# Performance work log

Hardware: AMD Instinct MI355X
Metric: run time of the kernel (lower is better)

Reference implementation:

```python
import jax, jax.numpy as jnp
import numpy as np

B, C, H, W = 8, 320, 32, 32
HEADS, DHEAD = 8, 40
CTX_LEN, CTX_DIM = 77, 768
FF_INNER = 4 * C
GROUPS = 32
HW = H * W


def setup_inputs() -> dict:
    key = jax.random.key(0)
    ks = jax.random.split(key, 16)
    def nrm(k, shape, s=0.02):
        return (jax.random.normal(k, shape) * s).astype(jnp.float32)
    z = lambda *s: jnp.zeros(s, jnp.float32)
    o = lambda *s: jnp.ones(s, jnp.float32)
    inp = {}
    inp["x"] = jax.random.normal(ks[0], (B, C, H, W), jnp.float32)
    inp["context"] = jax.random.normal(ks[1], (B, CTX_LEN, CTX_DIM), jnp.float32)
    inp["vis_mask"] = jax.random.uniform(ks[2], (B, HW, HW)) > 0.5
    inp["v2t_mask"] = jax.random.uniform(ks[3], (B, HW, CTX_LEN)) > 0.5
    inp["gn_scale"] = o(C); inp["gn_bias"] = z(C)
    inp["proj_in_w"] = nrm(ks[4], (C, C)); inp["proj_in_b"] = z(C)
    inp["n1_s"] = o(C); inp["n1_b"] = z(C)
    inp["wq1"] = nrm(ks[5], (C, C)); inp["wk1"] = nrm(ks[6], (C, C)); inp["wv1"] = nrm(ks[7], (C, C))
    inp["wo1"] = nrm(ks[8], (C, C)); inp["bo1"] = z(C)
    inp["n2_s"] = o(C); inp["n2_b"] = z(C)
    inp["wq2"] = nrm(ks[9], (C, C)); inp["wk2"] = nrm(ks[10], (CTX_DIM, C)); inp["wv2"] = nrm(ks[11], (CTX_DIM, C))
    inp["wo2"] = nrm(ks[12], (C, C)); inp["bo2"] = z(C)
    inp["n3_s"] = o(C); inp["n3_b"] = z(C)
    inp["ff_w1"] = nrm(ks[13], (C, 2 * FF_INNER)); inp["ff_b1"] = z(2 * FF_INNER)
    inp["ff_w2"] = nrm(ks[14], (FF_INNER, C)); inp["ff_b2"] = z(C)
    inp["proj_out_w"] = nrm(ks[15], (C, C)); inp["proj_out_b"] = z(C)
    return inp


def group_norm(x, scale, bias, eps=1e-6):
    b, c, h, w = x.shape
    xg = x.reshape(b, GROUPS, -1)
    mu = xg.mean(-1, keepdims=True)
    var = xg.var(-1, keepdims=True)
    xn = ((xg - mu) * jax.lax.rsqrt(var + eps)).reshape(b, c, h, w)
    return xn * scale[None, :, None, None] + bias[None, :, None, None]


def layer_norm(x, s, b, eps=1e-5):
    mu = x.mean(-1, keepdims=True)
    var = x.var(-1, keepdims=True)
    return (x - mu) * jax.lax.rsqrt(var + eps) * s + b


def mha(xq, ctx, wq, wk, wv, wo, bo, mask):
    # CrossAttention: manual einsum softmax with boolean mask broadcast over heads
    b, n, _ = xq.shape
    m = ctx.shape[1]
    split = lambda t: t.reshape(b, -1, HEADS, DHEAD).transpose(0, 2, 1, 3)
    q = split(xq @ wq)   # [b,h,n,d]
    k = split(ctx @ wk)  # [b,h,m,d]
    v = split(ctx @ wv)
    sim = jnp.einsum('bhid,bhjd->bhij', q, k) * (DHEAD ** -0.5)
    if mask is not None:
        sim = jnp.where(mask[:, None, :, :], sim, jnp.finfo(sim.dtype).min)
    attn = jax.nn.softmax(sim, axis=-1)
    out = jnp.einsum('bhij,bhjd->bhid', attn, v)
    out = out.transpose(0, 2, 1, 3).reshape(b, n, HEADS * DHEAD)
    return out @ wo + bo


def reference(x, context, vis_mask, v2t_mask, gn_scale, gn_bias, proj_in_w, proj_in_b,
              n1_s, n1_b, wq1, wk1, wv1, wo1, bo1,
              n2_s, n2_b, wq2, wk2, wv2, wo2, bo2,
              n3_s, n3_b, ff_w1, ff_b1, ff_w2, ff_b2,
              proj_out_w, proj_out_b):
    x_in = x
    h = group_norm(x, gn_scale, gn_bias)
    # 1x1 conv proj_in == per-pixel linear; flatten b c h w -> b (hw) c
    h = h.reshape(B, C, HW).transpose(0, 2, 1) @ proj_in_w + proj_in_b
    # masked self-attention (vis mask)
    h = h + mha(layer_norm(h, n1_s, n1_b), layer_norm(h, n1_s, n1_b),
                wq1, wk1, wv1, wo1, bo1, vis_mask)
    # masked cross-attention to text (v2t mask)
    h = h + mha(layer_norm(h, n2_s, n2_b), context,
                wq2, wk2, wv2, wo2, bo2, v2t_mask)
    # GEGLU feedforward (glu=True, mult=4)
    y = layer_norm(h, n3_s, n3_b) @ ff_w1 + ff_b1
    a, g = jnp.split(y, 2, axis=-1)
    h = h + (a * jax.nn.gelu(g, approximate=False)) @ ff_w2 + ff_b2
    # proj_out + residual
    out = (h @ proj_out_w + proj_out_b).transpose(0, 2, 1).reshape(B, C, H, W)
    return out + x_in
```

## Files before the change

kernel.cpp:

```cpp
#include <hip/hip_runtime.h>
#include <hip/hip_bf16.h>
#include <math.h>


#define Bsz   8
#define Cch   320
#define HW    1024
#define NTOK  (Bsz*HW)
#define HEADS 8
#define DHEAD 40
#define CTXL  77
#define CTXD  768
#define FFI   1280
#define MCTX  (Bsz*CTXL)
#define MCTXP 640

typedef unsigned short u16;
typedef unsigned long long u64;
typedef __attribute__((ext_vector_type(8))) u16    u16x8;
typedef __attribute__((ext_vector_type(8))) __bf16 bf16x8;
typedef __attribute__((ext_vector_type(4))) float  f32x4;

__device__ inline u16 f2b(float f) {
    unsigned u = __float_as_uint(f);
    return (u16)((u + 0x7FFFu + ((u >> 16) & 1u)) >> 16);
}

__global__ __launch_bounds__(256) void gn_stats(
    const float* __restrict__ x, const float* __restrict__ scale,
    const float* __restrict__ bias, float* __restrict__ gnA,
    float* __restrict__ gnB)
{
    int blk = blockIdx.x;
    int b = blk >> 5, g = blk & 31;
    int tid = threadIdx.x;
    __shared__ float rs[256], rq[256];
    const float4* xg = (const float4*)(x + ((size_t)b*Cch + g*10)*HW);
    float s = 0.f, q = 0.f;
    #pragma unroll
    for (int i = 0; i < 10; ++i) {
        float4 v = xg[tid + i*256];
        s += v.x + v.y + v.z + v.w;
        q += v.x*v.x + v.y*v.y + v.z*v.z + v.w*v.w;
    }
    rs[tid] = s; rq[tid] = q; __syncthreads();
    for (int off = 128; off > 0; off >>= 1) {
        if (tid < off) { rs[tid] += rs[tid+off]; rq[tid] += rq[tid+off]; }
        __syncthreads();
    }
    if (tid < 10) {
        float mean = rs[0] * (1.f/10240.f);
        float var  = rq[0] * (1.f/10240.f) - mean*mean;
        float inv  = rsqrtf(var + 1e-6f);
        int ch = g*10 + tid;
        float a = inv * scale[ch];
        gnA[b*Cch + ch] = a;
        gnB[b*Cch + ch] = bias[ch] - mean*a;
    }
}

__global__ __launch_bounds__(256) void gn_apply(
    const float* __restrict__ x, const float* __restrict__ gnA,
    const float* __restrict__ gnB, u16* __restrict__ out)
{
    __shared__ u16 T[64*72];
    const int tid = threadIdx.x;
    const int c0 = blockIdx.x * 64;
    const int p0 = blockIdx.y * 64;
    const int b  = blockIdx.z;
    for (int e = tid; e < 512; e += 256) {
        int r = e >> 3, ch = e & 7;
        const float* src = x + ((size_t)(b*Cch + c0 + r))*HW + p0 + ch*8;
        float a  = gnA[b*Cch + c0 + r];
        float bb = gnB[b*Cch + c0 + r];
        float4 v0 = *(const float4*)src;
        float4 v1 = *(const float4*)(src + 4);
        u16x8 val;
        val[0] = f2b(v0.x*a + bb); val[1] = f2b(v0.y*a + bb);
        val[2] = f2b(v0.z*a + bb); val[3] = f2b(v0.w*a + bb);
        val[4] = f2b(v1.x*a + bb); val[5] = f2b(v1.y*a + bb);
        val[6] = f2b(v1.z*a + bb); val[7] = f2b(v1.w*a + bb);
        *(u16x8*)&T[r*72 + (ch ^ (r & 7))*8] = val;
    }
    __syncthreads();
    for (int e = tid; e < 4096; e += 256) {
        int p = e >> 6, c = e & 63;
        u16 v = T[c*72 + (((p >> 3) ^ (c & 7))*8) + (p & 7)];
        out[((size_t)(b*HW + p0 + p))*Cch + c0 + c] = v;
    }
}

__global__ __launch_bounds__(256) void layernorm_kernel(
    const float* __restrict__ in, const float* __restrict__ s,
    const float* __restrict__ bgain, u16* __restrict__ out)
{
    int t = blockIdx.x*4 + (threadIdx.x >> 6);
    int lane = threadIdx.x & 63;
    const float* row = in + (size_t)t*Cch;
    float v[5];
    float sum = 0.f, sq = 0.f;
    #pragma unroll
    for (int i = 0; i < 5; ++i) {
        v[i] = row[lane + 64*i];
        sum += v[i]; sq += v[i]*v[i];
    }
    #pragma unroll
    for (int off = 32; off > 0; off >>= 1) {
        sum += __shfl_xor(sum, off);
        sq  += __shfl_xor(sq,  off);
    }
    float mean = sum * (1.f/320.f);
    float var  = sq  * (1.f/320.f) - mean*mean;
    float inv  = rsqrtf(var + 1e-5f);
    u16* orow = out + (size_t)t*Cch;
    #pragma unroll
    for (int i = 0; i < 5; ++i) {
        int c = lane + 64*i;
        orow[c] = f2b((v[i]-mean)*inv*s[c] + bgain[c]);
    }
}

struct WDesc { const float* src; u16* dst; int K; int N; int nelem; float scl; };
struct WPack { WDesc w[12]; };

#define WBLK 9920
#define CBLK 1920

__global__ __launch_bounds__(256) void preamble(
    WPack p, const float* __restrict__ ctxsrc, u16* __restrict__ ctxdst,
    const void* __restrict__ vis, const void* __restrict__ v2t,
    u64* __restrict__ bvis, u64* __restrict__ bv2t)
{
    int blk = blockIdx.x;
    int tid = threadIdx.x;
    if (blk < WBLK) {
        int idx = blk*256 + tid;
        #pragma unroll
        for (int i = 0; i < 12; ++i) {
            if (idx < p.w[i].nelem) {
                int K = p.w[i].K, N = p.w[i].N;
                int n = idx / K, k = idx - n*K;
                p.w[i].dst[(size_t)n*K + k] =
                    f2b(p.w[i].src[(size_t)k*N + n] * p.w[i].scl);
                return;
            }
            idx -= p.w[i].nelem;
        }
        return;
    }
    if (blk < WBLK + CBLK) {
        int idx = (blk - WBLK)*256 + tid;
        int r = idx / CTXD;
        float v = (r < MCTX) ? ctxsrc[idx] : 0.f;
        ctxdst[idx] = f2b(v);
        return;
    }
    __shared__ int any;
    if (tid == 0) any = 0;
    __syncthreads();
    const unsigned char* probe = (const unsigned char*)vis;
    for (int i = tid; i < 4096; i += 256)
        if ((i & 3) && probe[i]) any = 1;
    __syncthreads();
    const int isU8 = any;
    int mb = blk - WBLK - CBLK;
    const void* mask; u64* bits; int Lkv, nw;
    if (mb < 2048) { mask = vis; bits = bvis; Lkv = HW;   nw = 16; }
    else           { mask = v2t; bits = bv2t; Lkv = CTXL; nw = 2; mb -= 2048; }
    const int wv = tid >> 6, lane = tid & 63;
    const int row = mb*4 + wv;
    const unsigned char* m8  = (const unsigned char*)mask;
    const int*           m32 = (const int*)mask;
    const size_t base = (size_t)row * Lkv;
    for (int w = 0; w < nw; ++w) {
        int j = w*64 + lane;
        bool on = (j < Lkv) && (isU8 ? (m8[base+j] != 0) : (m32[base+j] != 0));
        u64 word = __ballot(on);
        if (lane == 0) bits[(size_t)row*nw + w] = word;
    }
}

__global__ __launch_bounds__(256) void gemm_bf16(
    const u16* __restrict__ A, const u16* __restrict__ Wt,
    const float* __restrict__ bias, const float* __restrict__ res,
    float* __restrict__ out, u16* __restrict__ out_bf, int M, int N, int K)
{
    __shared__ u16 As[2][128*40];
    __shared__ u16 Bs[2][64*40];
    const int tid  = threadIdx.x;
    const int lane = tid & 63;
    const int w    = tid >> 6;
    const int m0   = blockIdx.y * 128;
    const int n0   = blockIdx.x * 64;
    const int fr   = lane & 15, fg = lane >> 4;
    const int ar   = tid >> 2, ac = tid & 3;

    const u16* pa0 = A  + (size_t)(m0 + ar)*K      + ac*8;
    const u16* pa1 = A  + (size_t)(m0 + ar + 64)*K + ac*8;
    const u16* pb  = Wt + (size_t)(n0 + ar)*K      + ac*8;
    const int nk = K >> 5;

    *(u16x8*)&As[0][ar*40 + ac*8]      = *(const u16x8*)pa0;
    *(u16x8*)&As[0][(ar+64)*40 + ac*8] = *(const u16x8*)pa1;
    *(u16x8*)&Bs[0][ar*40 + ac*8]      = *(const u16x8*)pb;
    u16x8 ra0, ra1, rb;
    if (nk > 1) {
        pa0 += 32; pa1 += 32; pb += 32;
        ra0 = *(const u16x8*)pa0;
        ra1 = *(const u16x8*)pa1;
        rb  = *(const u16x8*)pb;
    }

    f32x4 acc[2][4] = {};
    for (int i = 0; i < nk; ++i) {
        __syncthreads();
        const int cur = i & 1;
        if (i + 1 < nk) {
            *(u16x8*)&As[cur^1][ar*40 + ac*8]      = ra0;
            *(u16x8*)&As[cur^1][(ar+64)*40 + ac*8] = ra1;
            *(u16x8*)&Bs[cur^1][ar*40 + ac*8]      = rb;
            if (i + 2 < nk) {
                pa0 += 32; pa1 += 32; pb += 32;
                ra0 = *(const u16x8*)pa0;
                ra1 = *(const u16x8*)pa1;
                rb  = *(const u16x8*)pb;
            }
        }
        bf16x8 a0 = *(const bf16x8*)&As[cur][(w*32      + fr)*40 + fg*8];
        bf16x8 a1 = *(const bf16x8*)&As[cur][(w*32 + 16 + fr)*40 + fg*8];
        #pragma unroll
        for (int nt = 0; nt < 4; ++nt) {
            bf16x8 b = *(const bf16x8*)&Bs[cur][(nt*16 + fr)*40 + fg*8];
            acc[0][nt] = __builtin_amdgcn_mfma_f32_16x16x32_bf16(a0, b, acc[0][nt], 0, 0, 0);
            acc[1][nt] = __builtin_amdgcn_mfma_f32_16x16x32_bf16(a1, b, acc[1][nt], 0, 0, 0);
        }
    }
    #pragma unroll
    for (int at = 0; at < 2; ++at) {
        #pragma unroll
        for (int nt = 0; nt < 4; ++nt) {
            int gn = n0 + nt*16 + fr;
            float bv = bias ? bias[gn] : 0.f;
            #pragma unroll
            for (int i = 0; i < 4; ++i) {
                int gm = m0 + w*32 + at*16 + fg*4 + i;
                float v = acc[at][nt][i] + bv;
                if (res) v += res[(size_t)gm*N + gn];
                if (out) out[(size_t)gm*N + gn] = v;
                if (out_bf) out_bf[(size_t)gm*N + gn] = f2b(v);
            }
        }
    }
}

__global__ __launch_bounds__(256) void gemm_pout(
    const u16* __restrict__ A, const u16* __restrict__ Wt,
    const float* __restrict__ bias, const float* __restrict__ x,
    float* __restrict__ out, int K)
{
    __shared__ u16 As[2][128*40];
    __shared__ u16 Bs[2][64*40];
    const int tid  = threadIdx.x;
    const int lane = tid & 63;
    const int w    = tid >> 6;
    const int m0   = blockIdx.y * 128;
    const int n0   = blockIdx.x * 64;
    const int fr   = lane & 15, fg = lane >> 4;
    const int ar   = tid >> 2, ac = tid & 3;

    const u16* pa0 = A  + (size_t)(m0 + ar)*K      + ac*8;
    const u16* pa1 = A  + (size_t)(m0 + ar + 64)*K + ac*8;
    const u16* pb  = Wt + (size_t)(n0 + ar)*K      + ac*8;
    const int nk = K >> 5;

    *(u16x8*)&As[0][ar*40 + ac*8]      = *(const u16x8*)pa0;
    *(u16x8*)&As[0][(ar+64)*40 + ac*8] = *(const u16x8*)pa1;
    *(u16x8*)&Bs[0][ar*40 + ac*8]      = *(const u16x8*)pb;
    u16x8 ra0, ra1, rb;
    if (nk > 1) {
        pa0 += 32; pa1 += 32; pb += 32;
        ra0 = *(const u16x8*)pa0;
        ra1 = *(const u16x8*)pa1;
        rb  = *(const u16x8*)pb;
    }

    f32x4 acc[2][4] = {};
    for (int i = 0; i < nk; ++i) {
        __syncthreads();
        const int cur = i & 1;
        if (i + 1 < nk) {
            *(u16x8*)&As[cur^1][ar*40 + ac*8]      = ra0;
            *(u16x8*)&As[cur^1][(ar+64)*40 + ac*8] = ra1;
            *(u16x8*)&Bs[cur^1][ar*40 + ac*8]      = rb;
            if (i + 2 < nk) {
                pa0 += 32; pa1 += 32; pb += 32;
                ra0 = *(const u16x8*)pa0;
                ra1 = *(const u16x8*)pa1;
                rb  = *(const u16x8*)pb;
            }
        }
        bf16x8 a0 = *(const bf16x8*)&As[cur][(w*32      + fr)*40 + fg*8];
        bf16x8 a1 = *(const bf16x8*)&As[cur][(w*32 + 16 + fr)*40 + fg*8];
        #pragma unroll
        for (int nt = 0; nt < 4; ++nt) {
            bf16x8 b = *(const bf16x8*)&Bs[cur][(nt*16 + fr)*40 + fg*8];
            acc[0][nt] = __builtin_amdgcn_mfma_f32_16x16x32_bf16(a0, b, acc[0][nt], 0, 0, 0);
            acc[1][nt] = __builtin_amdgcn_mfma_f32_16x16x32_bf16(a1, b, acc[1][nt], 0, 0, 0);
        }
    }
    #pragma unroll
    for (int at = 0; at < 2; ++at) {
        #pragma unroll
        for (int nt = 0; nt < 4; ++nt) {
            int gn = n0 + nt*16 + fr;
            float bv = bias[gn];
            int gm0 = m0 + w*32 + at*16 + fg*4;
            int b   = gm0 >> 10;
            int p   = gm0 & (HW-1);
            size_t o = ((size_t)(b*Cch + gn))*HW + p;
            f32x4 xv = *(const f32x4*)&x[o];
            f32x4 vv;
            #pragma unroll
            for (int i = 0; i < 4; ++i) vv[i] = acc[at][nt][i] + bv + xv[i];
            *(f32x4*)&out[o] = vv;
        }
    }
}

__global__ __launch_bounds__(256) void ctx_kv_gemm(
    const u16* __restrict__ ctx, const u16* __restrict__ wk,
    const u16* __restrict__ wv, u16* __restrict__ kout, u16* __restrict__ vout)
{
    __shared__ u16 As[2][64*40];
    __shared__ u16 Bs[2][64*40];
    const int tid  = threadIdx.x;
    const int lane = tid & 63;
    const int w    = tid >> 6;
    const int m0   = blockIdx.y * 64;
    const int n0   = blockIdx.x * 64;
    const u16* Wt  = blockIdx.z ? wv : wk;
    u16* outp      = blockIdx.z ? vout : kout;
    const int fr   = lane & 15, fg = lane >> 4;
    const int ar   = tid >> 2, ac = tid & 3;

    const u16* pa = ctx + (size_t)(m0 + ar)*CTXD + ac*8;
    const u16* pb = Wt  + (size_t)(n0 + ar)*CTXD + ac*8;
    const int nk = CTXD >> 5;

    *(u16x8*)&As[0][ar*40 + ac*8] = *(const u16x8*)pa;
    *(u16x8*)&Bs[0][ar*40 + ac*8] = *(const u16x8*)pb;
    u16x8 ra, rb;
    pa += 32; pb += 32;
    ra = *(const u16x8*)pa;
    rb = *(const u16x8*)pb;

    f32x4 acc[4] = {};
    for (int i = 0; i < nk; ++i) {
        __syncthreads();
        const int cur = i & 1;
        if (i + 1 < nk) {
            *(u16x8*)&As[cur^1][ar*40 + ac*8] = ra;
            *(u16x8*)&Bs[cur^1][ar*40 + ac*8] = rb;
            if (i + 2 < nk) {
                pa += 32; pb += 32;
                ra = *(const u16x8*)pa;
                rb = *(const u16x8*)pb;
            }
        }
        bf16x8 a = *(const bf16x8*)&As[cur][(w*16 + fr)*40 + fg*8];
        #pragma unroll
        for (int nt = 0; nt < 4; ++nt) {
            bf16x8 b = *(const bf16x8*)&Bs[cur][(nt*16 + fr)*40 + fg*8];
            acc[nt] = __builtin_amdgcn_mfma_f32_16x16x32_bf16(a, b, acc[nt], 0, 0, 0);
        }
    }
    #pragma unroll
    for (int nt = 0; nt < 4; ++nt) {
        int gn = n0 + nt*16 + fr;
        #pragma unroll
        for (int i = 0; i < 4; ++i) {
            int gm = m0 + w*16 + fg*4 + i;
            if (gm < MCTX)
                outp[(size_t)gm*Cch + gn] = f2b(acc[nt][i]);
        }
    }
}

__global__ __launch_bounds__(256) void geglu_bf16(
    const u16* __restrict__ A, const u16* __restrict__ Wt,
    const float* __restrict__ b1, u16* __restrict__ out, int M, int K)
{
    __shared__ u16 As[2][128*40];
    __shared__ u16 Ba[2][64*40];
    __shared__ u16 Bg[2][64*40];
    const int tid  = threadIdx.x;
    const int lane = tid & 63;
    const int w    = tid >> 6;
    const int m0   = blockIdx.y * 128;
    const int n0   = blockIdx.x * 64;
    const int fr   = lane & 15, fg = lane >> 4;
    const int ar   = tid >> 2, ac = tid & 3;

    const u16* pa0 = A  + (size_t)(m0 + ar)*K      + ac*8;
    const u16* pa1 = A  + (size_t)(m0 + ar + 64)*K + ac*8;
    const u16* pba = Wt + (size_t)(n0 + ar)*K       + ac*8;
    const u16* pbg = Wt + (size_t)(FFI + n0 + ar)*K + ac*8;
    const int nk = K >> 5;

    *(u16x8*)&As[0][ar*40 + ac*8]      = *(const u16x8*)pa0;
    *(u16x8*)&As[0][(ar+64)*40 + ac*8] = *(const u16x8*)pa1;
    *(u16x8*)&Ba[0][ar*40 + ac*8]      = *(const u16x8*)pba;
    *(u16x8*)&Bg[0][ar*40 + ac*8]      = *(const u16x8*)pbg;
    u16x8 ra0, ra1, rba, rbg;
    if (nk > 1) {
        pa0 += 32; pa1 += 32; pba += 32; pbg += 32;
        ra0 = *(const u16x8*)pa0;
        ra1 = *(const u16x8*)pa1;
        rba = *(const u16x8*)pba;
        rbg = *(const u16x8*)pbg;
    }

    f32x4 aca[2][4] = {}, acg[2][4] = {};
    for (int i = 0; i < nk; ++i) {
        __syncthreads();
        const int cur = i & 1;
        if (i + 1 < nk) {
            *(u16x8*)&As[cur^1][ar*40 + ac*8]      = ra0;
            *(u16x8*)&As[cur^1][(ar+64)*40 + ac*8] = ra1;
            *(u16x8*)&Ba[cur^1][ar*40 + ac*8]      = rba;
            *(u16x8*)&Bg[cur^1][ar*40 + ac*8]      = rbg;
            if (i + 2 < nk) {
                pa0 += 32; pa1 += 32; pba += 32; pbg += 32;
                ra0 = *(const u16x8*)pa0;
                ra1 = *(const u16x8*)pa1;
                rba = *(const u16x8*)pba;
                rbg = *(const u16x8*)pbg;
            }
        }
        bf16x8 a0 = *(const bf16x8*)&As[cur][(w*32      + fr)*40 + fg*8];
        bf16x8 a1 = *(const bf16x8*)&As[cur][(w*32 + 16 + fr)*40 + fg*8];
        #pragma unroll
        for (int nt = 0; nt < 4; ++nt) {
            bf16x8 ba = *(const bf16x8*)&Ba[cur][(nt*16 + fr)*40 + fg*8];
            bf16x8 bg = *(const bf16x8*)&Bg[cur][(nt*16 + fr)*40 + fg*8];
            aca[0][nt] = __builtin_amdgcn_mfma_f32_16x16x32_bf16(a0, ba, aca[0][nt], 0, 0, 0);
            aca[1][nt] = __builtin_amdgcn_mfma_f32_16x16x32_bf16(a1, ba, aca[1][nt], 0, 0, 0);
            acg[0][nt] = __builtin_amdgcn_mfma_f32_16x16x32_bf16(a0, bg, acg[0][nt], 0, 0, 0);
            acg[1][nt] = __builtin_amdgcn_mfma_f32_16x16x32_bf16(a1, bg, acg[1][nt], 0, 0, 0);
        }
    }
    #pragma unroll
    for (int at = 0; at < 2; ++at) {
        #pragma unroll
        for (int nt = 0; nt < 4; ++nt) {
            int gn = n0 + nt*16 + fr;
            float ba = b1[gn], bg = b1[FFI + gn];
            #pragma unroll
            for (int i = 0; i < 4; ++i) {
                int gm = m0 + w*32 + at*16 + fg*4 + i;
                float av = aca[at][nt][i] + ba;
                float gv = acg[at][nt][i] + bg;
                float gel = 0.5f*gv*(1.f + erff(gv*0.70710678118654752f));
                out[(size_t)gm*FFI + gn] = f2b(av*gel);
            }
        }
    }
}

__global__ __launch_bounds__(256) void transpose_v(
    const u16* __restrict__ in, int istride, u16* __restrict__ out,
    int Ltok, int ostride)
{
    __shared__ u16 T[64*72];
    const int tid = threadIdx.x;
    const int c0 = blockIdx.x * 64;
    const int t0 = blockIdx.y * 64;
    const int b  = blockIdx.z;
    for (int e = tid; e < 512; e += 256) {
        int r = e >> 3, ch = e & 7;
        u16x8 val = {};
        if (t0 + r < Ltok)
            val = *(const u16x8*)(in + ((size_t)(b*Ltok + t0 + r))*istride + c0 + ch*8);
        *(u16x8*)&T[r*72 + (ch ^ (r & 7))*8] = val;
    }
    __syncthreads();
    for (int e = tid; e < 4096; e += 256) {
        int c = e >> 6, t = e & 63;
        u16 v = T[t*72 + (((c >> 3) ^ (t & 7))*8) + (c & 7)];
        out[((size_t)(b*Cch + c0 + c))*ostride + t0 + t] = v;
    }
}

__global__ __launch_bounds__(256) void flash_mfma(
    const u16* __restrict__ qb, int qstride,
    const u16* __restrict__ kb, int kstride,
    const u16* __restrict__ vt, int vstride,
    const u64* __restrict__ mbits, int nw,
    u16* __restrict__ out,
    int Lkv)
{
    __shared__ u16 QPs[64*72];
    __shared__ u16 Ks[64*72];
    __shared__ u16 Vs[48*72];

    const int tid  = threadIdx.x;
    const int lane = tid & 63;
    const int w    = tid >> 6;
    const int col  = lane & 15;
    const int quad = lane >> 4;
    const int q0   = blockIdx.x * 64;
    const int h    = blockIdx.y;
    const int b    = blockIdx.z;
    const int ch   = tid & 7;
    const int r0   = tid >> 3;

    {
        const u16* qT = qb + ((size_t)(b*HW + q0))*qstride + (size_t)h*DHEAD + ch*8;
        u16x8 v0 = {}, v1 = {};
        if (ch < 5) {
            v0 = *(const u16x8*)(qT + (size_t)r0*qstride);
            v1 = *(const u16x8*)(qT + (size_t)(r0+32)*qstride);
        }
        *(u16x8*)&QPs[r0*72 + ch*8]      = v0;
        *(u16x8*)&QPs[(r0+32)*72 + ch*8] = v1;
    }
    __syncthreads();
    const bf16x8 qa0 = *(const bf16x8*)&QPs[(w*16 + col)*72 +  0 + quad*8];
    const bf16x8 qa1 = *(const bf16x8*)&QPs[(w*16 + col)*72 + 32 + quad*8];

    const u16* kT = kb + (size_t)b*Lkv*kstride + (size_t)h*DHEAD + ch*8;
    const bool kok = ch < 5;
    const u16* vT = vt + ((size_t)(b*Cch + h*DHEAD))*vstride + ch*8;
    const u64* mrow = mbits + ((size_t)(b*HW + q0 + w*16 + quad*4))*nw;

    f32x4 acc_o[3] = {};

    const int nkt = (Lkv + 63) / 64;
    for (int jt = 0; jt < nkt; ++jt) {
        const int j0 = jt*64;
        __syncthreads();
        {
            u16x8 v0 = {}, v1 = {};
            if (kok) {
                if (j0 + r0      < Lkv) v0 = *(const u16x8*)(kT + (size_t)(j0 + r0)*kstride);
                if (j0 + r0 + 32 < Lkv) v1 = *(const u16x8*)(kT + (size_t)(j0 + r0 + 32)*kstride);
            }
            *(u16x8*)&Ks[r0*72 + ch*8]      = v0;
            *(u16x8*)&Ks[(r0+32)*72 + ch*8] = v1;
        }
        {
            u16x8 v0 = {};
            if (r0 < DHEAD) v0 = *(const u16x8*)(vT + (size_t)r0*vstride + j0);
            *(u16x8*)&Vs[r0*72 + ch*8] = v0;
            if (tid < 128) {
                int d1 = 32 + (tid >> 3);
                u16x8 v1 = {};
                if (d1 < DHEAD) v1 = *(const u16x8*)(vT + (size_t)d1*vstride + j0);
                else if (d1 == DHEAD) {
                    #pragma unroll
                    for (int z = 0; z < 8; ++z) v1[z] = 0x3F80;
                }
                *(u16x8*)&Vs[d1*72 + ch*8] = v1;
            }
        }
        __syncthreads();

        u64 mw[4];
        #pragma unroll
        for (int i = 0; i < 4; ++i) mw[i] = mrow[i*nw + jt];

        f32x4 s[4] = {};
        #pragma unroll
        for (int nt = 0; nt < 4; ++nt) {
            bf16x8 b0 = *(const bf16x8*)&Ks[(nt*16 + col)*72 +  0 + quad*8];
            bf16x8 b1 = *(const bf16x8*)&Ks[(nt*16 + col)*72 + 32 + quad*8];
            s[nt] = __builtin_amdgcn_mfma_f32_16x16x32_bf16(qa0, b0, s[nt], 0, 0, 0);
            s[nt] = __builtin_amdgcn_mfma_f32_16x16x32_bf16(qa1, b1, s[nt], 0, 0, 0);
        }

        #pragma unroll
        for (int i = 0; i < 4; ++i) {
            #pragma unroll
            for (int nt = 0; nt < 4; ++nt) {
                float p = __expf(s[nt][i]);
                unsigned bits = (unsigned)(mw[i] >> (nt*16));
                s[nt][i] = ((bits >> col) & 1u) ? p : 0.f;
            }
        }

        #pragma unroll
        for (int nt = 0; nt < 4; ++nt)
            #pragma unroll
            for (int i = 0; i < 4; ++i)
                QPs[(w*16 + quad*4 + i)*68 + nt*16 + col] =
                    (u16)(__float_as_uint(s[nt][i]) >> 16);

        bf16x8 pa0, pa1;
        __builtin_memcpy(&pa0, &QPs[(w*16 + col)*68 +  0 + quad*8], 16);
        __builtin_memcpy(&pa1, &QPs[(w*16 + col)*68 + 32 + quad*8], 16);
        #pragma unroll
        for (int nt = 0; nt < 3; ++nt) {
            bf16x8 vb0 = *(const bf16x8*)&Vs[(nt*16 + col)*72 +  0 + quad*8];
            bf16x8 vb1 = *(const bf16x8*)&Vs[(nt*16 + col)*72 + 32 + quad*8];
            acc_o[nt] = __builtin_amdgcn_mfma_f32_16x16x32_bf16(pa0, vb0, acc_o[nt], 0, 0, 0);
            acc_o[nt] = __builtin_amdgcn_mfma_f32_16x16x32_bf16(pa1, vb1, acc_o[nt], 0, 0, 0);
        }
    }

    float inv_l[4];
    #pragma unroll
    for (int i = 0; i < 4; ++i)
        inv_l[i] = 1.f / __shfl(acc_o[2][i], (lane & 48) | 8);

    #pragma unroll
    for (int nt = 0; nt < 3; ++nt) {
        int d = nt*16 + col;
        if (d < DHEAD) {
            #pragma unroll
            for (int i = 0; i < 4; ++i) {
                int q = q0 + w*16 + quad*4 + i;
                out[((size_t)(b*HW + q))*Cch + h*DHEAD + d] = f2b(acc_o[nt][i] * inv_l[i]);
            }
        }
    }
}

extern "C" void kernel_launch(void* const* d_in, const int* in_sizes, int n_in,
                              void* d_out, int out_size, void* d_ws, size_t ws_size,
                              hipStream_t stream)
{
    const float* x        = (const float*)d_in[0];
    const float* context  = (const float*)d_in[1];
    const void*  vis_mask = d_in[2];
    const void*  v2t_mask = d_in[3];
    const float* gn_s     = (const float*)d_in[4];
    const float* gn_b     = (const float*)d_in[5];
    const float* proj_in_w= (const float*)d_in[6];
    const float* proj_in_b= (const float*)d_in[7];
    const float* n1_s     = (const float*)d_in[8];
    const float* n1_b     = (const float*)d_in[9];
    const float* wq1      = (const float*)d_in[10];
    const float* wk1      = (const float*)d_in[11];
    const float* wv1      = (const float*)d_in[12];
    const float* wo1      = (const float*)d_in[13];
    const float* bo1      = (const float*)d_in[14];
    const float* n2_s     = (const float*)d_in[15];
    const float* n2_b     = (const float*)d_in[16];
    const float* wq2      = (const float*)d_in[17];
    const float* wk2      = (const float*)d_in[18];
    const float* wv2      = (const float*)d_in[19];
    const float* wo2      = (const float*)d_in[20];
    const float* bo2      = (const float*)d_in[21];
    const float* n3_s     = (const float*)d_in[22];
    const float* n3_b     = (const float*)d_in[23];
    const float* ff_w1    = (const float*)d_in[24];
    const float* ff_b1    = (const float*)d_in[25];
    const float* ff_w2    = (const float*)d_in[26];
    const float* ff_b2    = (const float*)d_in[27];
    const float* pout_w   = (const float*)d_in[28];
    const float* pout_b   = (const float*)d_in[29];
    float* out = (float*)d_out;

    const size_t TOKC = (size_t)NTOK*Cch;
    float* ws   = (float*)d_ws;
    float* Hb   = ws;
    u16*   QKV  = (u16*)(Hb + TOKC);
    u16*   Vt_g = QKV + 3*TOKC;
    u16*   G_bf = QKV;
    u16*   T0b  = Vt_g + TOKC;
    u16*   T1b  = T0b + TOKC;
    u16*   Hb_bf= T1b + TOKC;
    u16*   Wbf  = Hb_bf + TOKC;
    u64*   mb_vis = (u64*)(Wbf + 2539520);
    u64*   mb_v2t = mb_vis + 131072;
    u16*   ctx_bf = (u16*)(mb_v2t + 16384);
    u16*   Kc_bf  = ctx_bf + MCTXP*CTXD;
    u16*   Vc_bf  = Kc_bf + 640*Cch;
    float* gnA    = (float*)(Vc_bf + 640*Cch);
    float* gnB    = gnA + Bsz*Cch;

    u16* w_q1  = Wbf;
    u16* w_k1  = Wbf +  102400;
    u16* w_v1  = Wbf +  204800;
    u16* w_pin = Wbf +  307200;
    u16* w_o1  = Wbf +  409600;
    u16* w_q2  = Wbf +  512000;
    u16* w_o2  = Wbf +  614400;
    u16* w_ff1 = Wbf +  716800;
    u16* w_ff2 = Wbf + 1536000;
    u16* w_po  = Wbf + 1945600;
    u16* w_k2  = Wbf + 2048000;
    u16* w_v2  = Wbf + 2293760;

    const float scale = 0.15811388300841897f;
    WPack pack;
    pack.w[0]  = { wq1,       w_q1,  Cch, Cch, Cch*Cch, scale };
    pack.w[1]  = { wk1,       w_k1,  Cch, Cch, Cch*Cch, 1.f };
    pack.w[2]  = { wv1,       w_v1,  Cch, Cch, Cch*Cch, 1.f };
    pack.w[3]  = { proj_in_w, w_pin, Cch, Cch, Cch*Cch, 1.f };
    pack.w[4]  = { wo1,       w_o1,  Cch, Cch, Cch*Cch, 1.f };
    pack.w[5]  = { wq2,       w_q2,  Cch, Cch, Cch*Cch, scale };
    pack.w[6]  = { wo2,       w_o2,  Cch, Cch, Cch*Cch, 1.f };
    pack.w[7]  = { ff_w1,     w_ff1, Cch, 2*FFI, Cch*2*FFI, 1.f };
    pack.w[8]  = { ff_w2,     w_ff2, FFI, Cch, FFI*Cch, 1.f };
    pack.w[9]  = { pout_w,    w_po,  Cch, Cch, Cch*Cch, 1.f };
    pack.w[10] = { wk2,       w_k2,  CTXD, Cch, CTXD*Cch, 1.f };
    pack.w[11] = { wv2,       w_v2,  CTXD, Cch, CTXD*Cch, 1.f };

    dim3 blk256(256);
    dim3 gTok(Cch/64, NTOK/128);
    dim3 gQKV(960/64, NTOK/128);
    dim3 gKV(Cch/64, MCTXP/64, 2);
    dim3 gFF(FFI/64, NTOK/128);
    dim3 gFA(HW/64, HEADS, Bsz);
    dim3 gTrS(Cch/64, HW/64, Bsz);
    dim3 gTrX(Cch/64, 2, Bsz);
    dim3 gGN(Cch/64, HW/64, Bsz);

    preamble<<<WBLK + CBLK + 4096, blk256, 0, stream>>>(
        pack, context, ctx_bf, vis_mask, v2t_mask, mb_vis, mb_v2t);

    gn_stats<<<Bsz*32, blk256, 0, stream>>>(x, gn_s, gn_b, gnA, gnB);
    gn_apply<<<gGN, blk256, 0, stream>>>(x, gnA, gnB, T0b);
    gemm_bf16<<<gTok, blk256, 0, stream>>>(T0b, w_pin, proj_in_b, nullptr, Hb, nullptr, NTOK, Cch, Cch);

    layernorm_kernel<<<NTOK/4, blk256, 0, stream>>>(Hb, n1_s, n1_b, T0b);
    gemm_bf16<<<gQKV, blk256, 0, stream>>>(T0b, w_q1, nullptr, nullptr, nullptr, QKV, NTOK, 960, Cch);
    transpose_v<<<gTrS, blk256, 0, stream>>>(QKV + 640, 960, Vt_g, HW, HW);
    flash_mfma<<<gFA, blk256, 0, stream>>>(QKV, 960, QKV + 320, 960, Vt_g, HW,
                                           mb_vis, 16, T1b, HW);
    gemm_bf16<<<gTok, blk256, 0, stream>>>(T1b, w_o1, bo1, Hb, Hb, nullptr, NTOK, Cch, Cch);

    layernorm_kernel<<<NTOK/4, blk256, 0, stream>>>(Hb, n2_s, n2_b, T0b);
    gemm_bf16<<<gTok, blk256, 0, stream>>>(T0b, w_q2, nullptr, nullptr, nullptr, QKV, NTOK, Cch, Cch);
    ctx_kv_gemm<<<gKV, blk256, 0, stream>>>(ctx_bf, w_k2, w_v2, Kc_bf, Vc_bf);
    transpose_v<<<gTrX, blk256, 0, stream>>>(Vc_bf, Cch, Vt_g, CTXL, 128);
    flash_mfma<<<gFA, blk256, 0, stream>>>(QKV, Cch, Kc_bf, Cch, Vt_g, 128,
                                           mb_v2t, 2, T1b, CTXL);
    gemm_bf16<<<gTok, blk256, 0, stream>>>(T1b, w_o2, bo2, Hb, Hb, nullptr, NTOK, Cch, Cch);

    layernorm_kernel<<<NTOK/4, blk256, 0, stream>>>(Hb, n3_s, n3_b, T0b);
    geglu_bf16<<<gFF, blk256, 0, stream>>>(T0b, w_ff1, ff_b1, G_bf, NTOK, Cch);
    gemm_bf16<<<gTok, blk256, 0, stream>>>(G_bf, w_ff2, ff_b2, Hb, nullptr, Hb_bf, NTOK, Cch, FFI);

    gemm_pout<<<gTok, blk256, 0, stream>>>(Hb_bf, w_po, pout_b, x, out, Cch);
}
```

Measured before the change: 408.1 us.

## Tile weight transpose through LDS, vectorize context cast, deepen GEMM prefetch

The preamble weight conversion now transposes 64x64 tiles through an XOR-swizzled shared-memory buffer. This replaces per-element strided global reads with coalesced float4 loads. The context-to-bf16 cast is vectorized to eight elements per thread. All GEMM kernels switch from one-ahead to two-ahead register prefetch of the next K slices. The change trades higher register pressure in the GEMMs for better latency hiding. The transpose stores remain 2-byte scalar writes, though each row's consecutive k values are now contiguous.

```diff
diff --git a/kernel.cpp b/kernel.cpp
--- a/kernel.cpp
+++ b/kernel.cpp
@@ -120,39 +120,69 @@
     }
 }
 
-struct WDesc { const float* src; u16* dst; int K; int N; int nelem; float scl; };
+struct WDesc { const float* src; u16* dst; int K; int N; int tiles; float scl; };
 struct WPack { WDesc w[12]; };
 
-#define WBLK 9920
-#define CBLK 1920
+#define WT_TILES 620
+#define CTXBLK   240
 
 __global__ __launch_bounds__(256) void preamble(
     WPack p, const float* __restrict__ ctxsrc, u16* __restrict__ ctxdst,
     const void* __restrict__ vis, const void* __restrict__ v2t,
     u64* __restrict__ bvis, u64* __restrict__ bv2t)
 {
+    __shared__ u16 T[64*72];
     int blk = blockIdx.x;
     int tid = threadIdx.x;
-    if (blk < WBLK) {
-        int idx = blk*256 + tid;
+    if (blk < WT_TILES) {
+        int t = blk;
         #pragma unroll
         for (int i = 0; i < 12; ++i) {
-            if (idx < p.w[i].nelem) {
-                int K = p.w[i].K, N = p.w[i].N;
-                int n = idx / K, k = idx - n*K;
-                p.w[i].dst[(size_t)n*K + k] =
-                    f2b(p.w[i].src[(size_t)k*N + n] * p.w[i].scl);
+            int nt = p.w[i].tiles;
+            if (t < nt) {
+                const int K = p.w[i].K, N = p.w[i].N;
+                const int ntN = N >> 6;
+                const int tk = t / ntN, tn = t - tk*ntN;
+                const float scl = p.w[i].scl;
+                const float* src = p.w[i].src;
+                u16* dst = p.w[i].dst;
+                for (int e = tid; e < 512; e += 256) {
+                    int r = e >> 3, ch = e & 7;
+                    const float* sp = src + (size_t)(tk*64 + r)*N + tn*64 + ch*8;
+                    float4 v0 = *(const float4*)sp;
+                    float4 v1 = *(const float4*)(sp + 4);
+                    u16x8 val;
+                    val[0] = f2b(v0.x*scl); val[1] = f2b(v0.y*scl);
+                    val[2] = f2b(v0.z*scl); val[3] = f2b(v0.w*scl);
+                    val[4] = f2b(v1.x*scl); val[5] = f2b(v1.y*scl);
+                    val[6] = f2b(v1.z*scl); val[7] = f2b(v1.w*scl);
+                    *(u16x8*)&T[r*72 + (ch ^ (r & 7))*8] = val;
+                }
+                __syncthreads();
+                for (int e = tid; e < 4096; e += 256) {
+                    int n = e >> 6, k = e & 63;
+                    u16 v = T[k*72 + (((n >> 3) ^ (k & 7))*8) + (n & 7)];
+                    dst[(size_t)(tn*64 + n)*K + tk*64 + k] = v;
+                }
                 return;
             }
-            idx -= p.w[i].nelem;
+            t -= nt;
         }
         return;
     }
-    if (blk < WBLK + CBLK) {
-        int idx = (blk - WBLK)*256 + tid;
+    if (blk < WT_TILES + CTXBLK) {
+        int idx = (blk - WT_TILES)*2048 + tid*8;
         int r = idx / CTXD;
-        float v = (r < MCTX) ? ctxsrc[idx] : 0.f;
-        ctxdst[idx] = f2b(v);
+        u16x8 val = {};
+        if (r < MCTX) {
+            float4 v0 = *(const float4*)(ctxsrc + idx);
+            float4 v1 = *(const float4*)(ctxsrc + idx + 4);
+            val[0] = f2b(v0.x); val[1] = f2b(v0.y);
+            val[2] = f2b(v0.z); val[3] = f2b(v0.w);
+            val[4] = f2b(v1.x); val[5] = f2b(v1.y);
+            val[6] = f2b(v1.z); val[7] = f2b(v1.w);
+        }
+        *(u16x8*)(ctxdst + idx) = val;
         return;
     }
     __shared__ int any;
@@ -163,7 +193,7 @@
         if ((i & 3) && probe[i]) any = 1;
     __syncthreads();
     const int isU8 = any;
-    int mb = blk - WBLK - CBLK;
+    int mb = blk - WT_TILES - CTXBLK;
     const void* mask; u64* bits; int Lkv, nw;
     if (mb < 2048) { mask = vis; bits = bvis; Lkv = HW;   nw = 16; }
     else           { mask = v2t; bits = bv2t; Lkv = CTXL; nw = 2; mb -= 2048; }
@@ -203,12 +233,16 @@
     *(u16x8*)&As[0][ar*40 + ac*8]      = *(const u16x8*)pa0;
     *(u16x8*)&As[0][(ar+64)*40 + ac*8] = *(const u16x8*)pa1;
     *(u16x8*)&Bs[0][ar*40 + ac*8]      = *(const u16x8*)pb;
-    u16x8 ra0, ra1, rb;
+    u16x8 ra0[2], ra1[2], rb[2];
     if (nk > 1) {
-        pa0 += 32; pa1 += 32; pb += 32;
-        ra0 = *(const u16x8*)pa0;
-        ra1 = *(const u16x8*)pa1;
-        rb  = *(const u16x8*)pb;
+        ra0[1] = *(const u16x8*)(pa0 + 32);
+        ra1[1] = *(const u16x8*)(pa1 + 32);
+        rb[1]  = *(const u16x8*)(pb  + 32);
+    }
+    if (nk > 2) {
+        ra0[0] = *(const u16x8*)(pa0 + 64);
+        ra1[0] = *(const u16x8*)(pa1 + 64);
+        rb[0]  = *(const u16x8*)(pb  + 64);
     }
 
     f32x4 acc[2][4] = {};
@@ -216,14 +250,15 @@
         __syncthreads();
         const int cur = i & 1;
         if (i + 1 < nk) {
-            *(u16x8*)&As[cur^1][ar*40 + ac*8]      = ra0;
-            *(u16x8*)&As[cur^1][(ar+64)*40 + ac*8] = ra1;
-            *(u16x8*)&Bs[cur^1][ar*40 + ac*8]      = rb;
-            if (i + 2 < nk) {
-                pa0 += 32; pa1 += 32; pb += 32;
-                ra0 = *(const u16x8*)pa0;
-                ra1 = *(const u16x8*)pa1;
-                rb  = *(const u16x8*)pb;
+            const int s = (i + 1) & 1;
+            *(u16x8*)&As[cur^1][ar*40 + ac*8]      = ra0[s];
+            *(u16x8*)&As[cur^1][(ar+64)*40 + ac*8] = ra1[s];
+            *(u16x8*)&Bs[cur^1][ar*40 + ac*8]      = rb[s];
+            if (i + 3 < nk) {
+                const int f = (i + 3) & 1;
+                ra0[f] = *(const u16x8*)(pa0 + 32*(i+3));
+                ra1[f] = *(const u16x8*)(pa1 + 32*(i+3));
+                rb[f]  = *(const u16x8*)(pb  + 32*(i+3));
             }
         }
         bf16x8 a0 = *(const bf16x8*)&As[cur][(w*32      + fr)*40 + fg*8];
@@ -276,12 +311,16 @@
     *(u16x8*)&As[0][ar*40 + ac*8]      = *(const u16x8*)pa0;
     *(u16x8*)&As[0][(ar+64)*40 + ac*8] = *(const u16x8*)pa1;
     *(u16x8*)&Bs[0][ar*40 + ac*8]      = *(const u16x8*)pb;
-    u16x8 ra0, ra1, rb;
+    u16x8 ra0[2], ra1[2], rb[2];
     if (nk > 1) {
-        pa0 += 32; pa1 += 32; pb += 32;
-        ra0 = *(const u16x8*)pa0;
-        ra1 = *(const u16x8*)pa1;
-        rb  = *(const u16x8*)pb;
+        ra0[1] = *(const u16x8*)(pa0 + 32);
+        ra1[1] = *(const u16x8*)(pa1 + 32);
+        rb[1]  = *(const u16x8*)(pb  + 32);
+    }
+    if (nk > 2) {
+        ra0[0] = *(const u16x8*)(pa0 + 64);
+        ra1[0] = *(const u16x8*)(pa1 + 64);
+        rb[0]  = *(const u16x8*)(pb  + 64);
     }
 
     f32x4 acc[2][4] = {};
@@ -289,14 +328,15 @@
         __syncthreads();
         const int cur = i & 1;
         if (i + 1 < nk) {
-            *(u16x8*)&As[cur^1][ar*40 + ac*8]      = ra0;
-            *(u16x8*)&As[cur^1][(ar+64)*40 + ac*8] = ra1;
-            *(u16x8*)&Bs[cur^1][ar*40 + ac*8]      = rb;
-            if (i + 2 < nk) {
-                pa0 += 32; pa1 += 32; pb += 32;
-                ra0 = *(const u16x8*)pa0;
-                ra1 = *(const u16x8*)pa1;
-                rb  = *(const u16x8*)pb;
+            const int s = (i + 1) & 1;
+            *(u16x8*)&As[cur^1][ar*40 + ac*8]      = ra0[s];
+            *(u16x8*)&As[cur^1][(ar+64)*40 + ac*8] = ra1[s];
+            *(u16x8*)&Bs[cur^1][ar*40 + ac*8]      = rb[s];
+            if (i + 3 < nk) {
+                const int f = (i + 3) & 1;
+                ra0[f] = *(const u16x8*)(pa0 + 32*(i+3));
+                ra1[f] = *(const u16x8*)(pa1 + 32*(i+3));
+                rb[f]  = *(const u16x8*)(pb  + 32*(i+3));
             }
         }
         bf16x8 a0 = *(const bf16x8*)&As[cur][(w*32      + fr)*40 + fg*8];
@@ -349,22 +389,24 @@
 
     *(u16x8*)&As[0][ar*40 + ac*8] = *(const u16x8*)pa;
     *(u16x8*)&Bs[0][ar*40 + ac*8] = *(const u16x8*)pb;
-    u16x8 ra, rb;
-    pa += 32; pb += 32;
-    ra = *(const u16x8*)pa;
-    rb = *(const u16x8*)pb;
+    u16x8 ra[2], rb[2];
+    ra[1] = *(const u16x8*)(pa + 32);
+    rb[1] = *(const u16x8*)(pb + 32);
+    ra[0] = *(const u16x8*)(pa + 64);
+    rb[0] = *(const u16x8*)(pb + 64);
 
     f32x4 acc[4] = {};
     for (int i = 0; i < nk; ++i) {
         __syncthreads();
         const int cur = i & 1;
         if (i + 1 < nk) {
-            *(u16x8*)&As[cur^1][ar*40 + ac*8] = ra;
-            *(u16x8*)&Bs[cur^1][ar*40 + ac*8] = rb;
-            if (i + 2 < nk) {
-                pa += 32; pb += 32;
-                ra = *(const u16x8*)pa;
-                rb = *(const u16x8*)pb;
+            const int s = (i + 1) & 1;
+            *(u16x8*)&As[cur^1][ar*40 + ac*8] = ra[s];
+            *(u16x8*)&Bs[cur^1][ar*40 + ac*8] = rb[s];
+            if (i + 3 < nk) {
+                const int f = (i + 3) & 1;
+                ra[f] = *(const u16x8*)(pa + 32*(i+3));
+                rb[f] = *(const u16x8*)(pb + 32*(i+3));
             }
         }
         bf16x8 a = *(const bf16x8*)&As[cur][(w*16 + fr)*40 + fg*8];
@@ -411,13 +453,18 @@
     *(u16x8*)&As[0][(ar+64)*40 + ac*8] = *(const u16x8*)pa1;
     *(u16x8*)&Ba[0][ar*40 + ac*8]      = *(const u16x8*)pba;
     *(u16x8*)&Bg[0][ar*40 + ac*8]      = *(const u16x8*)pbg;
-    u16x8 ra0, ra1, rba, rbg;
+    u16x8 ra0[2], ra1[2], rba[2], rbg[2];
     if (nk > 1) {
-        pa0 += 32; pa1 += 32; pba += 32; pbg += 32;
-        ra0 = *(const u16x8*)pa0;
-        ra1 = *(const u16x8*)pa1;
-        rba = *(const u16x8*)pba;
-        rbg = *(const u16x8*)pbg;
+        ra0[1] = *(const u16x8*)(pa0 + 32);
+        ra1[1] = *(const u16x8*)(pa1 + 32);
+        rba[1] = *(const u16x8*)(pba + 32);
+        rbg[1] = *(const u16x8*)(pbg + 32);
+    }
+    if (nk > 2) {
+        ra0[0] = *(const u16x8*)(pa0 + 64);
+        ra1[0] = *(const u16x8*)(pa1 + 64);
+        rba[0] = *(const u16x8*)(pba + 64);
+        rbg[0] = *(const u16x8*)(pbg + 64);
     }
 
     f32x4 aca[2][4] = {}, acg[2][4] = {};
@@ -425,16 +472,17 @@
         __syncthreads();
         const int cur = i & 1;
         if (i + 1 < nk) {
-            *(u16x8*)&As[cur^1][ar*40 + ac*8]      = ra0;
-            *(u16x8*)&As[cur^1][(ar+64)*40 + ac*8] = ra1;
-            *(u16x8*)&Ba[cur^1][ar*40 + ac*8]      = rba;
-            *(u16x8*)&Bg[cur^1][ar*40 + ac*8]      = rbg;
-            if (i + 2 < nk) {
-                pa0 += 32; pa1 += 32; pba += 32; pbg += 32;
-                ra0 = *(const u16x8*)pa0;
-                ra1 = *(const u16x8*)pa1;
-                rba = *(const u16x8*)pba;
-                rbg = *(const u16x8*)pbg;
+            const int s = (i + 1) & 1;
+            *(u16x8*)&As[cur^1][ar*40 + ac*8]      = ra0[s];
+            *(u16x8*)&As[cur^1][(ar+64)*40 + ac*8] = ra1[s];
+            *(u16x8*)&Ba[cur^1][ar*40 + ac*8]      = rba[s];
+            *(u16x8*)&Bg[cur^1][ar*40 + ac*8]      = rbg[s];
+            if (i + 3 < nk) {
+                const int f = (i + 3) & 1;
+                ra0[f] = *(const u16x8*)(pa0 + 32*(i+3));
+                ra1[f] = *(const u16x8*)(pa1 + 32*(i+3));
+                rba[f] = *(const u16x8*)(pba + 32*(i+3));
+                rbg[f] = *(const u16x8*)(pbg + 32*(i+3));
             }
         }
         bf16x8 a0 = *(const bf16x8*)&As[cur][(w*32      + fr)*40 + fg*8];
@@ -694,18 +742,18 @@
 
     const float scale = 0.15811388300841897f;
     WPack pack;
-    pack.w[0]  = { wq1,       w_q1,  Cch, Cch, Cch*Cch, scale };
-    pack.w[1]  = { wk1,       w_k1,  Cch, Cch, Cch*Cch, 1.f };
-    pack.w[2]  = { wv1,       w_v1,  Cch, Cch, Cch*Cch, 1.f };
-    pack.w[3]  = { proj_in_w, w_pin, Cch, Cch, Cch*Cch, 1.f };
-    pack.w[4]  = { wo1,       w_o1,  Cch, Cch, Cch*Cch, 1.f };
-    pack.w[5]  = { wq2,       w_q2,  Cch, Cch, Cch*Cch, scale };
-    pack.w[6]  = { wo2,       w_o2,  Cch, Cch, Cch*Cch, 1.f };
-    pack.w[7]  = { ff_w1,     w_ff1, Cch, 2*FFI, Cch*2*FFI, 1.f };
-    pack.w[8]  = { ff_w2,     w_ff2, FFI, Cch, FFI*Cch, 1.f };
-    pack.w[9]  = { pout_w,    w_po,  Cch, Cch, Cch*Cch, 1.f };
-    pack.w[10] = { wk2,       w_k2,  CTXD, Cch, CTXD*Cch, 1.f };
-    pack.w[11] = { wv2,       w_v2,  CTXD, Cch, CTXD*Cch, 1.f };
+    pack.w[0]  = { wq1,       w_q1,  Cch, Cch, 25,  scale };
+    pack.w[1]  = { wk1,       w_k1,  Cch, Cch, 25,  1.f };
+    pack.w[2]  = { wv1,       w_v1,  Cch, Cch, 25,  1.f };
+    pack.w[3]  = { proj_in_w, w_pin, Cch, Cch, 25,  1.f };
+    pack.w[4]  = { wo1,       w_o1,  Cch, Cch, 25,  1.f };
+    pack.w[5]  = { wq2,       w_q2,  Cch, Cch, 25,  scale };
+    pack.w[6]  = { wo2,       w_o2,  Cch, Cch, 25,  1.f };
+    pack.w[7]  = { ff_w1,     w_ff1, Cch, 2*FFI, 200, 1.f };
+    pack.w[8]  = { ff_w2,     w_ff2, FFI, Cch, 100, 1.f };
+    pack.w[9]  = { pout_w,    w_po,  Cch, Cch, 25,  1.f };
+    pack.w[10] = { wk2,       w_k2,  CTXD, Cch, 60, 1.f };
+    pack.w[11] = { wv2,       w_v2,  CTXD, Cch, 60, 1.f };
 
     dim3 blk256(256);
     dim3 gTok(Cch/64, NTOK/128);
@@ -717,7 +765,7 @@
     dim3 gTrX(Cch/64, 2, Bsz);
     dim3 gGN(Cch/64, HW/64, Bsz);
 
-    preamble<<<WBLK + CBLK + 4096, blk256, 0, stream>>>(
+    preamble<<<WT_TILES + CTXBLK + 4096, blk256, 0, stream>>>(
         pack, context, ctx_bf, vis_mask, v2t_mask, mb_vis, mb_v2t);
 
     gn_stats<<<Bsz*32, blk256, 0, stream>>>(x, gn_s, gn_b, gnA, gnB);
```

Result: slower. 805.6 us (+97.4%).
